# Kernel tuning notes

Measured on AMD Instinct MI355X. Metric: run time of the kernel, lower is better.

## Reference

```python
import jax, jax.numpy as jnp
import numpy as np

N_NODES = 100000


def _graph_conv(x, W, b, src, dst, norm):
    # DGL GraphConv(norm='left'): scale source features by 1/out_degree,
    # aggregate (sum over incoming edges). in_feats > out_feats so weight
    # multiply happens before aggregation (mathematically equivalent either way).
    h = x @ W  # [N, out]
    msg = (h * norm[:, None])[src]  # gather per-edge messages [E, out]
    agg = jax.ops.segment_sum(msg, dst, num_segments=N_NODES)
    return agg + b


def setup_inputs() -> dict:
    key = jax.random.key(0)
    ks = jax.random.split(key, 10)
    in_f, hid_f, out_f = 256, 128, 64
    n_edges = 1_600_000
    feat = jax.random.normal(ks[0], (N_NODES, in_f), dtype=jnp.float32)
    src = jax.random.randint(ks[1], (n_edges,), 0, N_NODES, dtype=jnp.int32)
    dst = jax.random.randint(ks[2], (n_edges,), 0, N_NODES, dtype=jnp.int32)
    noise = jax.random.normal(ks[3], (N_NODES, out_f), dtype=jnp.float32)
    s1 = 1.0 / np.sqrt(in_f)
    s2 = 1.0 / np.sqrt(hid_f)
    W_shared = jax.random.uniform(ks[4], (in_f, hid_f), minval=-s1, maxval=s1, dtype=jnp.float32)
    b_shared = jnp.zeros((hid_f,), jnp.float32)
    W_mu = jax.random.uniform(ks[5], (hid_f, out_f), minval=-s2, maxval=s2, dtype=jnp.float32)
    b_mu = jnp.zeros((out_f,), jnp.float32)
    W_ls = jax.random.uniform(ks[6], (hid_f, out_f), minval=-s2, maxval=s2, dtype=jnp.float32)
    b_ls = jnp.zeros((out_f,), jnp.float32)
    return {"feat": feat, "W_shared": W_shared, "b_shared": b_shared,
            "W_mu": W_mu, "b_mu": b_mu, "W_ls": W_ls, "b_ls": b_ls,
            "noise": noise, "src": src, "dst": dst}


def reference(feat, W_shared, b_shared, W_mu, b_mu, W_ls, b_ls, noise, src, dst):
    # left-norm: 1 / out_degree (clamped to >= 1, as DGL does)
    deg_out = jax.ops.segment_sum(jnp.ones_like(src, jnp.float32), src,
                                  num_segments=N_NODES)
    norm = 1.0 / jnp.maximum(deg_out, 1.0)
    # shared first GraphConv with ReLU activation
    h = jax.nn.relu(_graph_conv(feat, W_shared, b_shared, src, dst, norm))
    # two heads (no activation)
    mu = _graph_conv(h, W_mu, b_mu, src, dst, norm)
    log_sigma = _graph_conv(h, W_ls, b_ls, src, dst, norm)
    # reparameterized sample
    return mu + noise * jnp.exp(log_sigma)
```

## Files before the change

### kernel.cpp

```cpp
#include <hip/hip_runtime.h>
#include <hip/hip_bf16.h>
#include <math.h>

typedef __attribute__((ext_vector_type(8))) short short8;
typedef __attribute__((ext_vector_type(4))) float f32x4;

__device__ __forceinline__ unsigned short f2bf(float f) {
    unsigned int u = __float_as_uint(f);
    u += 0x7FFF + ((u >> 16) & 1);
    return (unsigned short)(u >> 16);
}
__device__ __forceinline__ float b2f(unsigned short s) {
    return __uint_as_float(((unsigned int)s) << 16);
}
__device__ __forceinline__ unsigned int f2bf2(float a, float b) {
    __hip_bfloat162 h = __float22bfloat162_rn(make_float2(a, b));
    return *(unsigned int*)&h;
}
__device__ __forceinline__ void gl_lds16(const void* g, void* l) {
    __builtin_amdgcn_global_load_lds(
        (const __attribute__((address_space(1))) void*)g,
        (__attribute__((address_space(3))) void*)l, 16, 0, 0);
}

#define EB 2048
#define SH 9
#define BSZ 512

__global__ __launch_bounds__(256)
void k1_hist(const int* __restrict__ src, const int* __restrict__ dst,
             int* __restrict__ bhist, int E, int NB2) {
    __shared__ int hist[512];
    int t = threadIdx.x;
    int NB = NB2 >> 1;
    for (int i = t; i < NB2; i += 256) hist[i] = 0;
    __syncthreads();
    int base = blockIdx.x * EB;
    int end = min(base + EB, E);
    for (int e = base + 4 * t; e < end; e += 1024) {
        if (e + 3 < end) {
            int4 d4 = *(const int4*)&dst[e];
            int4 s4 = *(const int4*)&src[e];
            atomicAdd(&hist[d4.x >> SH], 1);
            atomicAdd(&hist[d4.y >> SH], 1);
            atomicAdd(&hist[d4.z >> SH], 1);
            atomicAdd(&hist[d4.w >> SH], 1);
            atomicAdd(&hist[NB + (s4.x >> SH)], 1);
            atomicAdd(&hist[NB + (s4.y >> SH)], 1);
            atomicAdd(&hist[NB + (s4.z >> SH)], 1);
            atomicAdd(&hist[NB + (s4.w >> SH)], 1);
        } else {
            for (int q = e; q < end; ++q) {
                atomicAdd(&hist[dst[q] >> SH], 1);
                atomicAdd(&hist[NB + (src[q] >> SH)], 1);
            }
        }
    }
    __syncthreads();
    for (int i = t; i < NB2; i += 256)
        bhist[(size_t)blockIdx.x * NB2 + i] = hist[i];
}

__global__ __launch_bounds__(512)
void kc1_totals(const int* __restrict__ bhist, int* __restrict__ totals,
                int PB, int NB2) {
    int t = threadIdx.x;
    if (t >= NB2) return;
    int slice = (PB + 15) / 16;
    int b0 = blockIdx.x * slice;
    int b1 = min(b0 + slice, PB);
    int s = 0;
    for (int blk = b0; blk < b1; ++blk) s += bhist[(size_t)blk * NB2 + t];
    if (s) atomicAdd(&totals[t], s);
}

__global__ __launch_bounds__(512)
void kc2_scan(const int* __restrict__ totals, int* __restrict__ bbase, int NB) {
    __shared__ int s[512];
    int t = threadIdx.x;
    int half = t >> 8;
    int idx = t & 255;
    int v = (idx < NB) ? totals[half * NB + idx] : 0;
    s[t] = v;
    __syncthreads();
    for (int off = 1; off < 256; off <<= 1) {
        int u = (idx >= off) ? s[t - off] : 0;
        __syncthreads();
        s[t] += u;
        __syncthreads();
    }
    if (idx < NB) bbase[half * NB + idx] = s[t] - v;
}

__global__ __launch_bounds__(1024)
void kc3_boff(const int* __restrict__ bhist, const int* __restrict__ bbase,
              int* __restrict__ boffT, int PB, int NB2) {
    __shared__ int sums[1024];
    int b = blockIdx.x;
    int t = threadIdx.x;
    int v = (t < PB) ? bhist[(size_t)t * NB2 + b] : 0;
    sums[t] = v;
    __syncthreads();
    for (int off = 1; off < 1024; off <<= 1) {
        int u = (t >= off) ? sums[t - off] : 0;
        __syncthreads();
        sums[t] += u;
        __syncthreads();
    }
    if (t < PB) boffT[(size_t)b * PB + t] = bbase[b] + sums[t] - v;
}

__global__ __launch_bounds__(256)
void k2_scatter(const int* __restrict__ src, const int* __restrict__ dst,
                const int* __restrict__ boffT, int* __restrict__ parr,
                unsigned short* __restrict__ sarr, int E, int PB, int NB2) {
    __shared__ int cnt[512];
    int t = threadIdx.x;
    int blk = blockIdx.x;
    int NB = NB2 >> 1;
    for (int i = t; i < NB2; i += 256) cnt[i] = boffT[(size_t)i * PB + blk];
    __syncthreads();
    int base = blk * EB;
    int end = min(base + EB, E);
    for (int e = base + 4 * t; e < end; e += 1024) {
        if (e + 3 < end) {
            int4 s4 = *(const int4*)&src[e];
            int4 d4 = *(const int4*)&dst[e];
            int p0 = atomicAdd(&cnt[d4.x >> SH], 1);
            parr[p0] = (s4.x << SH) | (d4.x & (BSZ - 1));
            int p1 = atomicAdd(&cnt[d4.y >> SH], 1);
            parr[p1] = (s4.y << SH) | (d4.y & (BSZ - 1));
            int p2 = atomicAdd(&cnt[d4.z >> SH], 1);
            parr[p2] = (s4.z << SH) | (d4.z & (BSZ - 1));
            int p3 = atomicAdd(&cnt[d4.w >> SH], 1);
            parr[p3] = (s4.w << SH) | (d4.w & (BSZ - 1));
            int q0 = atomicAdd(&cnt[NB + (s4.x >> SH)], 1);
            sarr[q0] = (unsigned short)(s4.x & (BSZ - 1));
            int q1 = atomicAdd(&cnt[NB + (s4.y >> SH)], 1);
            sarr[q1] = (unsigned short)(s4.y & (BSZ - 1));
            int q2 = atomicAdd(&cnt[NB + (s4.z >> SH)], 1);
            sarr[q2] = (unsigned short)(s4.z & (BSZ - 1));
            int q3 = atomicAdd(&cnt[NB + (s4.w >> SH)], 1);
            sarr[q3] = (unsigned short)(s4.w & (BSZ - 1));
        } else {
            for (int q = e; q < end; ++q) {
                int sv = src[q], dv = dst[q];
                int pd = atomicAdd(&cnt[dv >> SH], 1);
                parr[pd] = (sv << SH) | (dv & (BSZ - 1));
                int ps = atomicAdd(&cnt[NB + (sv >> SH)], 1);
                sarr[ps] = (unsigned short)(sv & (BSZ - 1));
            }
        }
    }
}

__global__ __launch_bounds__(1024)
void k3_dst(const int* __restrict__ parr, const int* __restrict__ totals,
            const int* __restrict__ bbase, int* __restrict__ row_off,
            int* __restrict__ col, int N, int E) {
    __shared__ int hist[512], sc[512];
    int b = blockIdx.x, t = threadIdx.x;
    if (b == 0 && t == 0) row_off[N] = E;
    int ne = totals[b];
    int ebase = bbase[b];
    if (t < 512) hist[t] = 0;
    __syncthreads();
    for (int i = t; i < ne; i += 1024)
        atomicAdd(&hist[parr[ebase + i] & (BSZ - 1)], 1);
    __syncthreads();
    int h = 0;
    if (t < 512) { h = hist[t]; sc[t] = h; }
    __syncthreads();
    for (int off = 1; off < 512; off <<= 1) {
        int u = (t < 512 && t >= off) ? sc[t - off] : 0;
        __syncthreads();
        if (t < 512) sc[t] += u;
        __syncthreads();
    }
    if (t < 512) {
        int excl = sc[t] - h;
        int node = b * BSZ + t;
        if (node < N) row_off[node] = ebase + excl;
        hist[t] = ebase + excl;
    }
    __syncthreads();
    for (int i = t; i < ne; i += 1024) {
        int pr = parr[ebase + i];
        int slot = atomicAdd(&hist[pr & (BSZ - 1)], 1);
        col[slot] = pr >> SH;
    }
}

__global__ __launch_bounds__(1024)
void k3_src(const unsigned short* __restrict__ sarr, const int* __restrict__ totals_s,
            const int* __restrict__ bbase_s, float* __restrict__ norm, int N) {
    __shared__ int hist[512];
    int b = blockIdx.x, t = threadIdx.x;
    int ne = totals_s[b];
    int sb = bbase_s[b];
    if (t < 512) hist[t] = 0;
    __syncthreads();
    for (int i = t; i < ne; i += 1024)
        atomicAdd(&hist[sarr[sb + i]], 1);
    __syncthreads();
    int node = b * BSZ + t;
    if (t < 512 && node < N) {
        int d = hist[t];
        norm[node] = 1.0f / (float)(d > 1 ? d : 1);
    }
}


__global__ __launch_bounds__(256)
void k_wprep(const float* __restrict__ Wsh, const float* __restrict__ Wmu,
             const float* __restrict__ Wls, unsigned short* __restrict__ W1T,
             unsigned short* __restrict__ W2T) {
    int b = blockIdx.x, t = threadIdx.x;
    if (b < 128) {
        W1T[(size_t)b * 256 + t] = f2bf(Wsh[(size_t)t * 128 + b]);
    } else {
        int n = b - 128;
        if (t < 128) {
            float v = (n < 64) ? Wmu[(size_t)t * 64 + n]
                               : Wls[(size_t)t * 64 + (n - 64)];
            W2T[(size_t)n * 128 + t] = f2bf(v);
        }
    }
}

__global__ __launch_bounds__(256)
void k_gemm1(const float* __restrict__ A, int M,
             const unsigned short* __restrict__ W1T,
             const float* __restrict__ norm, unsigned short* __restrict__ outb) {
    __shared__ char ldsA[64 * 1040];
    const int w = threadIdx.x >> 6;
    const int lane = threadIdx.x & 63;
    const int quad = lane >> 4;
    const int l16 = lane & 15;
    const int cl = w * 16 + l16;
    const int r0 = blockIdx.x * 64;

#pragma unroll
    for (int i = 0; i < 16; ++i) {
        int row = r0 + w * 16 + i;
        if (row >= M) row = M - 1;
        const char* g = (const char*)A + (size_t)row * 1024 + lane * 16;
        char* l = ldsA + (w * 16 + i) * 1040 + lane * 16;
        gl_lds16(g, l);
    }

    short8 bw[2][8];
#pragma unroll
    for (int hf = 0; hf < 2; ++hf) {
        const unsigned short* wp = W1T + (size_t)(hf * 64 + cl) * 256 + quad * 8;
#pragma unroll
        for (int ks = 0; ks < 8; ++ks)
            bw[hf][ks] = *(const short8*)(wp + ks * 32);
    }
    __syncthreads();

    f32x4 acc[4][2];
#pragma unroll
    for (int m = 0; m < 4; ++m) {
        acc[m][0] = (f32x4){0.f, 0.f, 0.f, 0.f};
        acc[m][1] = (f32x4){0.f, 0.f, 0.f, 0.f};
    }
#pragma unroll
    for (int ks = 0; ks < 8; ++ks) {
#pragma unroll
        for (int m = 0; m < 4; ++m) {
            const float* pr = (const float*)(ldsA + (m * 16 + l16) * 1040 +
                                             (ks * 32 + quad * 8) * 4);
            float4 x = *(const float4*)pr;
            float4 y = *(const float4*)(pr + 4);
            union { short8 v; unsigned int u[4]; } c;
            c.u[0] = f2bf2(x.x, x.y);
            c.u[1] = f2bf2(x.z, x.w);
            c.u[2] = f2bf2(y.x, y.y);
            c.u[3] = f2bf2(y.z, y.w);
            acc[m][0] = __builtin_amdgcn_mfma_f32_16x16x32_bf16(bw[0][ks], c.v, acc[m][0], 0, 0, 0);
            acc[m][1] = __builtin_amdgcn_mfma_f32_16x16x32_bf16(bw[1][ks], c.v, acc[m][1], 0, 0, 0);
        }
    }
    const int colbase = w * 16 + quad * 4;
#pragma unroll
    for (int m = 0; m < 4; ++m) {
        int row = r0 + m * 16 + l16;
        if (row < M) {
            float nm = norm[row];
            ushort4 o0, o1;
            o0.x = f2bf(acc[m][0][0] * nm); o0.y = f2bf(acc[m][0][1] * nm);
            o0.z = f2bf(acc[m][0][2] * nm); o0.w = f2bf(acc[m][0][3] * nm);
            o1.x = f2bf(acc[m][1][0] * nm); o1.y = f2bf(acc[m][1][1] * nm);
            o1.z = f2bf(acc[m][1][2] * nm); o1.w = f2bf(acc[m][1][3] * nm);
            *(ushort4*)&outb[(size_t)row * 128 + colbase] = o0;
            *(ushort4*)&outb[(size_t)row * 128 + 64 + colbase] = o1;
        }
    }
}

__global__ __launch_bounds__(256)
void k_gemm2(const unsigned short* __restrict__ A, int M,
             const unsigned short* __restrict__ W2T,
             const float* __restrict__ norm, unsigned short* __restrict__ outb) {
    __shared__ char ldsB[16 * 1040];
    const int w = threadIdx.x >> 6;
    const int lane = threadIdx.x & 63;
    const int quad = lane >> 4;
    const int l16 = lane & 15;
    const int cl = w * 16 + l16;
    const int r0 = blockIdx.x * 64;

#pragma unroll
    for (int i = 0; i < 4; ++i) {
        int c = w * 4 + i;
        int crow = r0 + c * 4;
        if (crow + 4 > M) crow = M - 4;
        const char* g = (const char*)A + (size_t)crow * 256 + lane * 16;
        char* l = ldsB + c * 1040 + lane * 16;
        gl_lds16(g, l);
    }

    short8 bw[2][4];
#pragma unroll
    for (int hf = 0; hf < 2; ++hf) {
        const unsigned short* wp = W2T + (size_t)(hf * 64 + cl) * 128 + quad * 8;
#pragma unroll
        for (int ks = 0; ks < 4; ++ks)
            bw[hf][ks] = *(const short8*)(wp + ks * 32);
    }
    __syncthreads();

    f32x4 acc[4][2];
#pragma unroll
    for (int m = 0; m < 4; ++m) {
        acc[m][0] = (f32x4){0.f, 0.f, 0.f, 0.f};
        acc[m][1] = (f32x4){0.f, 0.f, 0.f, 0.f};
    }
#pragma unroll
    for (int ks = 0; ks < 4; ++ks) {
#pragma unroll
        for (int m = 0; m < 4; ++m) {
            int row = m * 16 + l16;
            short8 af = *(const short8*)(ldsB + (row >> 2) * 1040 + (row & 3) * 256 +
                                         (ks * 32 + quad * 8) * 2);
            acc[m][0] = __builtin_amdgcn_mfma_f32_16x16x32_bf16(bw[0][ks], af, acc[m][0], 0, 0, 0);
            acc[m][1] = __builtin_amdgcn_mfma_f32_16x16x32_bf16(bw[1][ks], af, acc[m][1], 0, 0, 0);
        }
    }
    const int colbase = w * 16 + quad * 4;
#pragma unroll
    for (int m = 0; m < 4; ++m) {
        int row = r0 + m * 16 + l16;
        if (row < M) {
            float nm = norm[row];
            ushort4 o0, o1;
            o0.x = f2bf(acc[m][0][0] * nm); o0.y = f2bf(acc[m][0][1] * nm);
            o0.z = f2bf(acc[m][0][2] * nm); o0.w = f2bf(acc[m][0][3] * nm);
            o1.x = f2bf(acc[m][1][0] * nm); o1.y = f2bf(acc[m][1][1] * nm);
            o1.z = f2bf(acc[m][1][2] * nm); o1.w = f2bf(acc[m][1][3] * nm);
            *(ushort4*)&outb[(size_t)row * 128 + colbase] = o0;
            *(ushort4*)&outb[(size_t)row * 128 + 64 + colbase] = o1;
        }
    }
}

__global__ __launch_bounds__(256)
void k_spmm_relu(const int* __restrict__ row_off, const int* __restrict__ col,
                 const unsigned short* __restrict__ hxb, const float* __restrict__ bias,
                 unsigned short* __restrict__ hb, int N) {
    int g = (blockIdx.x * blockDim.x + threadIdx.x) >> 5;
    int l = threadIdx.x & 31;
    if (g >= N) return;
    int e0 = row_off[g], e1 = row_off[g + 1];
    const ushort4* base = (const ushort4*)hxb;
    float4 acc = make_float4(0.f, 0.f, 0.f, 0.f);
    int e = e0;
    for (; e + 7 < e1; e += 8) {
        ushort4 v0 = base[(size_t)col[e] * 32 + l];
        ushort4 v1 = base[(size_t)col[e + 1] * 32 + l];
        ushort4 v2 = base[(size_t)col[e + 2] * 32 + l];
        ushort4 v3 = base[(size_t)col[e + 3] * 32 + l];
        ushort4 v4 = base[(size_t)col[e + 4] * 32 + l];
        ushort4 v5 = base[(size_t)col[e + 5] * 32 + l];
        ushort4 v6 = base[(size_t)col[e + 6] * 32 + l];
        ushort4 v7 = base[(size_t)col[e + 7] * 32 + l];
        acc.x += ((b2f(v0.x) + b2f(v1.x)) + (b2f(v2.x) + b2f(v3.x))) +
                 ((b2f(v4.x) + b2f(v5.x)) + (b2f(v6.x) + b2f(v7.x)));
        acc.y += ((b2f(v0.y) + b2f(v1.y)) + (b2f(v2.y) + b2f(v3.y))) +
                 ((b2f(v4.y) + b2f(v5.y)) + (b2f(v6.y) + b2f(v7.y)));
        acc.z += ((b2f(v0.z) + b2f(v1.z)) + (b2f(v2.z) + b2f(v3.z))) +
                 ((b2f(v4.z) + b2f(v5.z)) + (b2f(v6.z) + b2f(v7.z)));
        acc.w += ((b2f(v0.w) + b2f(v1.w)) + (b2f(v2.w) + b2f(v3.w))) +
                 ((b2f(v4.w) + b2f(v5.w)) + (b2f(v6.w) + b2f(v7.w)));
    }
    for (; e + 1 < e1; e += 2) {
        ushort4 a = base[(size_t)col[e] * 32 + l];
        ushort4 b = base[(size_t)col[e + 1] * 32 + l];
        acc.x += b2f(a.x) + b2f(b.x);
        acc.y += b2f(a.y) + b2f(b.y);
        acc.z += b2f(a.z) + b2f(b.z);
        acc.w += b2f(a.w) + b2f(b.w);
    }
    if (e < e1) {
        ushort4 a = base[(size_t)col[e] * 32 + l];
        acc.x += b2f(a.x); acc.y += b2f(a.y); acc.z += b2f(a.z); acc.w += b2f(a.w);
    }
    float4 bi = ((const float4*)bias)[l];
    ushort4 r;
    r.x = f2bf(fmaxf(acc.x + bi.x, 0.f));
    r.y = f2bf(fmaxf(acc.y + bi.y, 0.f));
    r.z = f2bf(fmaxf(acc.z + bi.z, 0.f));
    r.w = f2bf(fmaxf(acc.w + bi.w, 0.f));
    ((ushort4*)hb)[(size_t)g * 32 + l] = r;
}

__global__ __launch_bounds__(256)
void k_spmm_out(const int* __restrict__ row_off, const int* __restrict__ col,
                const unsigned short* __restrict__ hcb, const float* __restrict__ bmu,
                const float* __restrict__ bls, const float* __restrict__ noise,
                float* __restrict__ out, int N) {
    int g = (blockIdx.x * blockDim.x + threadIdx.x) >> 5;
    int l = threadIdx.x & 31;
    if (g >= N) return;
    int e0 = row_off[g], e1 = row_off[g + 1];
    const ushort4* base = (const ushort4*)hcb;
    float4 acc = make_float4(0.f, 0.f, 0.f, 0.f);
    int e = e0;
    for (; e + 7 < e1; e += 8) {
        ushort4 v0 = base[(size_t)col[e] * 32 + l];
        ushort4 v1 = base[(size_t)col[e + 1] * 32 + l];
        ushort4 v2 = base[(size_t)col[e + 2] * 32 + l];
        ushort4 v3 = base[(size_t)col[e + 3] * 32 + l];
        ushort4 v4 = base[(size_t)col[e + 4] * 32 + l];
        ushort4 v5 = base[(size_t)col[e + 5] * 32 + l];
        ushort4 v6 = base[(size_t)col[e + 6] * 32 + l];
        ushort4 v7 = base[(size_t)col[e + 7] * 32 + l];
        acc.x += ((b2f(v0.x) + b2f(v1.x)) + (b2f(v2.x) + b2f(v3.x))) +
                 ((b2f(v4.x) + b2f(v5.x)) + (b2f(v6.x) + b2f(v7.x)));
        acc.y += ((b2f(v0.y) + b2f(v1.y)) + (b2f(v2.y) + b2f(v3.y))) +
                 ((b2f(v4.y) + b2f(v5.y)) + (b2f(v6.y) + b2f(v7.y)));
        acc.z += ((b2f(v0.z) + b2f(v1.z)) + (b2f(v2.z) + b2f(v3.z))) +
                 ((b2f(v4.z) + b2f(v5.z)) + (b2f(v6.z) + b2f(v7.z)));
        acc.w += ((b2f(v0.w) + b2f(v1.w)) + (b2f(v2.w) + b2f(v3.w))) +
                 ((b2f(v4.w) + b2f(v5.w)) + (b2f(v6.w) + b2f(v7.w)));
    }
    for (; e + 1 < e1; e += 2) {
        ushort4 a = base[(size_t)col[e] * 32 + l];
        ushort4 b = base[(size_t)col[e + 1] * 32 + l];
        acc.x += b2f(a.x) + b2f(b.x);
        acc.y += b2f(a.y) + b2f(b.y);
        acc.z += b2f(a.z) + b2f(b.z);
        acc.w += b2f(a.w) + b2f(b.w);
    }
    if (e < e1) {
        ushort4 a = base[(size_t)col[e] * 32 + l];
        acc.x += b2f(a.x); acc.y += b2f(a.y); acc.z += b2f(a.z); acc.w += b2f(a.w);
    }
    int lane64 = threadIdx.x & 63;
    int p = (lane64 + 16) & 63;
    float lx = __shfl(acc.x, p, 64);
    float ly = __shfl(acc.y, p, 64);
    float lz = __shfl(acc.z, p, 64);
    float lw = __shfl(acc.w, p, 64);
    if (l < 16) {
        float4 bm = ((const float4*)bmu)[l];
        float4 bl = ((const float4*)bls)[l];
        float4 nz = ((const float4*)noise)[(size_t)g * 16 + l];
        float4 o;
        o.x = (acc.x + bm.x) + nz.x * expf(lx + bl.x);
        o.y = (acc.y + bm.y) + nz.y * expf(ly + bl.y);
        o.z = (acc.z + bm.z) + nz.z * expf(lz + bl.z);
        o.w = (acc.w + bm.w) + nz.w * expf(lw + bl.w);
        ((float4*)out)[(size_t)g * 16 + l] = o;
    }
}

static inline char* align64(char* p) {
    return (char*)(((uintptr_t)p + 63) & ~(uintptr_t)63);
}

extern "C" void kernel_launch(void* const* d_in, const int* in_sizes, int n_in,
                              void* d_out, int out_size, void* d_ws, size_t ws_size,
                              hipStream_t stream) {
    const float* feat  = (const float*)d_in[0];
    const float* Wsh   = (const float*)d_in[1];
    const float* bsh   = (const float*)d_in[2];
    const float* Wmu   = (const float*)d_in[3];
    const float* bmu   = (const float*)d_in[4];
    const float* Wls   = (const float*)d_in[5];
    const float* bls   = (const float*)d_in[6];
    const float* noise = (const float*)d_in[7];
    const int*   src   = (const int*)d_in[8];
    const int*   dst   = (const int*)d_in[9];
    float* out = (float*)d_out;

    const int N = in_sizes[0] / 256;
    const int E = in_sizes[8];
    const int PB = (E + EB - 1) / EB;
    const int NB = (N + BSZ - 1) / BSZ;
    const int NB2 = 2 * NB;

    char* p = (char*)d_ws;
    float* norm   = (float*)p;                  p += (size_t)N * 4;          p = align64(p);
    int* row_off  = (int*)p;                    p += (size_t)(N + 4) * 4;    p = align64(p);
    int* totals   = (int*)p;                    p += 512 * 4;
    int* bbase    = (int*)p;                    p += 512 * 4;                p = align64(p);
    unsigned short* W1T = (unsigned short*)p;   p += (size_t)128 * 256 * 2;
    unsigned short* W2T = (unsigned short*)p;   p += (size_t)128 * 128 * 2;
    p = align64(p);
    int* bhist    = (int*)p;                    p += (size_t)PB * NB2 * 4;   p = align64(p);
    int* boffT    = (int*)p;                    p += (size_t)NB2 * PB * 4;   p = align64(p);
    int* parr     = (int*)p;                    p += (size_t)E * 4;
    unsigned short* sarr = (unsigned short*)p;  p += (size_t)E * 2;          p = align64(p);
    int* col      = (int*)p;                    p += (size_t)E * 4;          p = align64(p);
    unsigned short* hxb = (unsigned short*)p;
    unsigned short* hb  = (unsigned short*)d_out;

    hipMemsetAsync(totals, 0, 512 * sizeof(int), stream);
    k_wprep<<<256, 256, 0, stream>>>(Wsh, Wmu, Wls, W1T, W2T);
    k1_hist<<<PB, 256, 0, stream>>>(src, dst, bhist, E, NB2);
    kc1_totals<<<16, 512, 0, stream>>>(bhist, totals, PB, NB2);
    kc2_scan<<<1, 512, 0, stream>>>(totals, bbase, NB);
    kc3_boff<<<NB2, 1024, 0, stream>>>(bhist, bbase, boffT, PB, NB2);
    k2_scatter<<<PB, 256, 0, stream>>>(src, dst, boffT, parr, sarr, E, PB, NB2);
    k3_dst<<<NB, 1024, 0, stream>>>(parr, totals, bbase, row_off, col, N, E);
    k3_src<<<NB, 1024, 0, stream>>>(sarr, totals + NB, bbase + NB, norm, N);

    int gtiles = (N + 63) / 64;
    k_gemm1<<<gtiles, 256, 0, stream>>>(feat, N, W1T, norm, hxb);
    k_spmm_relu<<<(N * 32 + 255) / 256, 256, 0, stream>>>(row_off, col, hxb, bsh, hb, N);
    k_gemm2<<<gtiles, 256, 0, stream>>>(hb, N, W2T, norm, hxb);
    k_spmm_out<<<(N * 32 + 255) / 256, 256, 0, stream>>>(row_off, col, hxb, bmu, bls, noise, out, N);
}
```

Baseline: 444.6 us.

## Fuse second aggregation with head GEMM and merge CSR build kernels

The second-layer pipeline changes order: the norm scaling moves into the ReLU aggregation, and a new fused kernel gathers neighbor rows of the normalized hidden features into LDS, then multiplies by the stacked head weights with MFMA and applies the reparameterization epilogue. This drops the separate GEMM2 pass and the round trip of its output through memory, at the cost of aggregating 128-wide rows instead of projecting first. Separately, the scan kernel and memset are folded into existing kernels (redundant per-block scans of the totals), and the dst/src CSR finalization kernels are merged into one launch. A fallback path keeps the old three-kernel sequence when the workspace is too small.

```diff
diff --git a/kernel.cpp b/kernel.cpp
--- a/kernel.cpp
+++ b/kernel.cpp
@@ -74,30 +74,24 @@
     if (s) atomicAdd(&totals[t], s);
 }
 
-__global__ __launch_bounds__(512)
-void kc2_scan(const int* __restrict__ totals, int* __restrict__ bbase, int NB) {
-    __shared__ int s[512];
-    int t = threadIdx.x;
-    int half = t >> 8;
-    int idx = t & 255;
-    int v = (idx < NB) ? totals[half * NB + idx] : 0;
-    s[t] = v;
-    __syncthreads();
-    for (int off = 1; off < 256; off <<= 1) {
-        int u = (idx >= off) ? s[t - off] : 0;
-        __syncthreads();
-        s[t] += u;
-        __syncthreads();
-    }
-    if (idx < NB) bbase[half * NB + idx] = s[t] - v;
-}
-
 __global__ __launch_bounds__(1024)
-void kc3_boff(const int* __restrict__ bhist, const int* __restrict__ bbase,
-              int* __restrict__ boffT, int PB, int NB2) {
+void kc3_boff(const int* __restrict__ bhist, const int* __restrict__ totals,
+              int* __restrict__ boffT, int PB, int NB) {
     __shared__ int sums[1024];
+    __shared__ int tb[512];
     int b = blockIdx.x;
     int t = threadIdx.x;
+    int NB2 = 2 * NB;
+    if (t < 512) tb[t] = (t < NB2) ? totals[t] : 0;
+    __syncthreads();
+    for (int off = 1; off < 512; off <<= 1) {
+        int u = (t < 512 && t >= off) ? tb[t - off] : 0;
+        __syncthreads();
+        if (t < 512) tb[t] += u;
+        __syncthreads();
+    }
+    int lo = (b < NB) ? 0 : NB;
+    int base = ((b > lo) ? tb[b - 1] : 0) - ((lo > 0 && b > lo) ? tb[lo - 1] : 0);
     int v = (t < PB) ? bhist[(size_t)t * NB2 + b] : 0;
     sums[t] = v;
     __syncthreads();
@@ -107,7 +101,7 @@
         sums[t] += u;
         __syncthreads();
     }
-    if (t < PB) boffT[(size_t)b * PB + t] = bbase[b] + sums[t] - v;
+    if (t < PB) boffT[(size_t)b * PB + t] = base + sums[t] - v;
 }
 
 __global__ __launch_bounds__(256)
@@ -155,58 +149,66 @@
 }
 
 __global__ __launch_bounds__(1024)
-void k3_dst(const int* __restrict__ parr, const int* __restrict__ totals,
-            const int* __restrict__ bbase, int* __restrict__ row_off,
-            int* __restrict__ col, int N, int E) {
+void k3_both(const int* __restrict__ parr, const unsigned short* __restrict__ sarr,
+             const int* __restrict__ totals, int* __restrict__ row_off,
+             int* __restrict__ col, float* __restrict__ norm,
+             int N, int E, int NB) {
     __shared__ int hist[512], sc[512];
+    __shared__ int tb[512];
     int b = blockIdx.x, t = threadIdx.x;
-    if (b == 0 && t == 0) row_off[N] = E;
-    int ne = totals[b];
-    int ebase = bbase[b];
-    if (t < 512) hist[t] = 0;
-    __syncthreads();
-    for (int i = t; i < ne; i += 1024)
-        atomicAdd(&hist[parr[ebase + i] & (BSZ - 1)], 1);
-    __syncthreads();
-    int h = 0;
-    if (t < 512) { h = hist[t]; sc[t] = h; }
+    int NB2 = 2 * NB;
+    if (t < 512) tb[t] = (t < NB2) ? totals[t] : 0;
     __syncthreads();
     for (int off = 1; off < 512; off <<= 1) {
-        int u = (t < 512 && t >= off) ? sc[t - off] : 0;
-        __syncthreads();
-        if (t < 512) sc[t] += u;
-        __syncthreads();
-    }
-    if (t < 512) {
-        int excl = sc[t] - h;
-        int node = b * BSZ + t;
-        if (node < N) row_off[node] = ebase + excl;
-        hist[t] = ebase + excl;
-    }
-    __syncthreads();
-    for (int i = t; i < ne; i += 1024) {
-        int pr = parr[ebase + i];
-        int slot = atomicAdd(&hist[pr & (BSZ - 1)], 1);
-        col[slot] = pr >> SH;
-    }
-}
-
-__global__ __launch_bounds__(1024)
-void k3_src(const unsigned short* __restrict__ sarr, const int* __restrict__ totals_s,
-            const int* __restrict__ bbase_s, float* __restrict__ norm, int N) {
-    __shared__ int hist[512];
-    int b = blockIdx.x, t = threadIdx.x;
-    int ne = totals_s[b];
-    int sb = bbase_s[b];
-    if (t < 512) hist[t] = 0;
-    __syncthreads();
-    for (int i = t; i < ne; i += 1024)
-        atomicAdd(&hist[sarr[sb + i]], 1);
-    __syncthreads();
-    int node = b * BSZ + t;
-    if (t < 512 && node < N) {
-        int d = hist[t];
-        norm[node] = 1.0f / (float)(d > 1 ? d : 1);
+        int u = (t < 512 && t >= off) ? tb[t - off] : 0;
+        __syncthreads();
+        if (t < 512) tb[t] += u;
+        __syncthreads();
+    }
+    if (b < NB) {
+        if (b == 0 && t == 0) row_off[N] = E;
+        int ne = totals[b];
+        int ebase = (b > 0) ? tb[b - 1] : 0;
+        if (t < 512) hist[t] = 0;
+        __syncthreads();
+        for (int i = t; i < ne; i += 1024)
+            atomicAdd(&hist[parr[ebase + i] & (BSZ - 1)], 1);
+        __syncthreads();
+        int h = 0;
+        if (t < 512) { h = hist[t]; sc[t] = h; }
+        __syncthreads();
+        for (int off = 1; off < 512; off <<= 1) {
+            int u = (t < 512 && t >= off) ? sc[t - off] : 0;
+            __syncthreads();
+            if (t < 512) sc[t] += u;
+            __syncthreads();
+        }
+        if (t < 512) {
+            int excl = sc[t] - h;
+            int node = b * BSZ + t;
+            if (node < N) row_off[node] = ebase + excl;
+            hist[t] = ebase + excl;
+        }
+        __syncthreads();
+        for (int i = t; i < ne; i += 1024) {
+            int pr = parr[ebase + i];
+            int slot = atomicAdd(&hist[pr & (BSZ - 1)], 1);
+            col[slot] = pr >> SH;
+        }
+    } else {
+        int bs = b - NB;
+        int ne = totals[NB + bs];
+        int sbase = (bs > 0) ? (tb[b - 1] - tb[NB - 1]) : 0;
+        if (t < 512) hist[t] = 0;
+        __syncthreads();
+        for (int i = t; i < ne; i += 1024)
+            atomicAdd(&hist[sarr[sbase + i]], 1);
+        __syncthreads();
+        int node = bs * BSZ + t;
+        if (t < 512 && node < N) {
+            int d = hist[t];
+            norm[node] = 1.0f / (float)(d > 1 ? d : 1);
+        }
     }
 }
 
@@ -214,8 +216,9 @@
 __global__ __launch_bounds__(256)
 void k_wprep(const float* __restrict__ Wsh, const float* __restrict__ Wmu,
              const float* __restrict__ Wls, unsigned short* __restrict__ W1T,
-             unsigned short* __restrict__ W2T) {
+             unsigned short* __restrict__ W2T, int* __restrict__ totals) {
     int b = blockIdx.x, t = threadIdx.x;
+    if (b == 0) { totals[t] = 0; totals[256 + t] = 0; }
     if (b < 128) {
         W1T[(size_t)b * 256 + t] = f2bf(Wsh[(size_t)t * 128 + b]);
     } else {
@@ -299,81 +302,11 @@
     }
 }
 
-__global__ __launch_bounds__(256)
-void k_gemm2(const unsigned short* __restrict__ A, int M,
-             const unsigned short* __restrict__ W2T,
-             const float* __restrict__ norm, unsigned short* __restrict__ outb) {
-    __shared__ char ldsB[16 * 1040];
-    const int w = threadIdx.x >> 6;
-    const int lane = threadIdx.x & 63;
-    const int quad = lane >> 4;
-    const int l16 = lane & 15;
-    const int cl = w * 16 + l16;
-    const int r0 = blockIdx.x * 64;
-
-#pragma unroll
-    for (int i = 0; i < 4; ++i) {
-        int c = w * 4 + i;
-        int crow = r0 + c * 4;
-        if (crow + 4 > M) crow = M - 4;
-        const char* g = (const char*)A + (size_t)crow * 256 + lane * 16;
-        char* l = ldsB + c * 1040 + lane * 16;
-        gl_lds16(g, l);
-    }
-
-    short8 bw[2][4];
-#pragma unroll
-    for (int hf = 0; hf < 2; ++hf) {
-        const unsigned short* wp = W2T + (size_t)(hf * 64 + cl) * 128 + quad * 8;
-#pragma unroll
-        for (int ks = 0; ks < 4; ++ks)
-            bw[hf][ks] = *(const short8*)(wp + ks * 32);
-    }
-    __syncthreads();
-
-    f32x4 acc[4][2];
-#pragma unroll
-    for (int m = 0; m < 4; ++m) {
-        acc[m][0] = (f32x4){0.f, 0.f, 0.f, 0.f};
-        acc[m][1] = (f32x4){0.f, 0.f, 0.f, 0.f};
-    }
-#pragma unroll
-    for (int ks = 0; ks < 4; ++ks) {
-#pragma unroll
-        for (int m = 0; m < 4; ++m) {
-            int row = m * 16 + l16;
-            short8 af = *(const short8*)(ldsB + (row >> 2) * 1040 + (row & 3) * 256 +
-                                         (ks * 32 + quad * 8) * 2);
-            acc[m][0] = __builtin_amdgcn_mfma_f32_16x16x32_bf16(bw[0][ks], af, acc[m][0], 0, 0, 0);
-            acc[m][1] = __builtin_amdgcn_mfma_f32_16x16x32_bf16(bw[1][ks], af, acc[m][1], 0, 0, 0);
-        }
-    }
-    const int colbase = w * 16 + quad * 4;
-#pragma unroll
-    for (int m = 0; m < 4; ++m) {
-        int row = r0 + m * 16 + l16;
-        if (row < M) {
-            float nm = norm[row];
-            ushort4 o0, o1;
-            o0.x = f2bf(acc[m][0][0] * nm); o0.y = f2bf(acc[m][0][1] * nm);
-            o0.z = f2bf(acc[m][0][2] * nm); o0.w = f2bf(acc[m][0][3] * nm);
-            o1.x = f2bf(acc[m][1][0] * nm); o1.y = f2bf(acc[m][1][1] * nm);
-            o1.z = f2bf(acc[m][1][2] * nm); o1.w = f2bf(acc[m][1][3] * nm);
-            *(ushort4*)&outb[(size_t)row * 128 + colbase] = o0;
-            *(ushort4*)&outb[(size_t)row * 128 + 64 + colbase] = o1;
-        }
-    }
-}
-
-__global__ __launch_bounds__(256)
-void k_spmm_relu(const int* __restrict__ row_off, const int* __restrict__ col,
-                 const unsigned short* __restrict__ hxb, const float* __restrict__ bias,
-                 unsigned short* __restrict__ hb, int N) {
-    int g = (blockIdx.x * blockDim.x + threadIdx.x) >> 5;
-    int l = threadIdx.x & 31;
-    if (g >= N) return;
+__device__ __forceinline__ float4 gather_row(const int* __restrict__ row_off,
+                                             const int* __restrict__ col,
+                                             const ushort4* __restrict__ base,
+                                             int g, int l) {
     int e0 = row_off[g], e1 = row_off[g + 1];
-    const ushort4* base = (const ushort4*)hxb;
     float4 acc = make_float4(0.f, 0.f, 0.f, 0.f);
     int e = e0;
     for (; e + 7 < e1; e += 8) {
@@ -406,13 +339,160 @@
         ushort4 a = base[(size_t)col[e] * 32 + l];
         acc.x += b2f(a.x); acc.y += b2f(a.y); acc.z += b2f(a.z); acc.w += b2f(a.w);
     }
+    return acc;
+}
+
+__global__ __launch_bounds__(256)
+void k_spmm_relu(const int* __restrict__ row_off, const int* __restrict__ col,
+                 const unsigned short* __restrict__ hxb, const float* __restrict__ bias,
+                 const float* __restrict__ norm, unsigned short* __restrict__ hb, int N) {
+    int g = (blockIdx.x * blockDim.x + threadIdx.x) >> 5;
+    int l = threadIdx.x & 31;
+    if (g >= N) return;
+    float4 acc = gather_row(row_off, col, (const ushort4*)hxb, g, l);
     float4 bi = ((const float4*)bias)[l];
+    float nm = norm[g];
     ushort4 r;
-    r.x = f2bf(fmaxf(acc.x + bi.x, 0.f));
-    r.y = f2bf(fmaxf(acc.y + bi.y, 0.f));
-    r.z = f2bf(fmaxf(acc.z + bi.z, 0.f));
-    r.w = f2bf(fmaxf(acc.w + bi.w, 0.f));
+    r.x = f2bf(fmaxf(acc.x + bi.x, 0.f) * nm);
+    r.y = f2bf(fmaxf(acc.y + bi.y, 0.f) * nm);
+    r.z = f2bf(fmaxf(acc.z + bi.z, 0.f) * nm);
+    r.w = f2bf(fmaxf(acc.w + bi.w, 0.f) * nm);
     ((ushort4*)hb)[(size_t)g * 32 + l] = r;
+}
+
+__global__ __launch_bounds__(512)
+void k_spmm_gemm_out(const int* __restrict__ row_off, const int* __restrict__ col,
+                     const unsigned short* __restrict__ hnb,
+                     const unsigned short* __restrict__ W2T,
+                     const float* __restrict__ bmu, const float* __restrict__ bls,
+                     const float* __restrict__ noise, float* __restrict__ out, int N) {
+    __shared__ char ldsB[16 * 1040];
+    const int tid = threadIdx.x;
+    const int r0 = blockIdx.x * 64;
+    const int hw = tid >> 5;
+    const int l = tid & 31;
+    const ushort4* base = (const ushort4*)hnb;
+#pragma unroll
+    for (int it = 0; it < 4; ++it) {
+        int lrow = hw + 16 * it;
+        int g = r0 + lrow;
+        float4 acc = make_float4(0.f, 0.f, 0.f, 0.f);
+        if (g < N) acc = gather_row(row_off, col, base, g, l);
+        ushort4 r;
+        r.x = f2bf(acc.x); r.y = f2bf(acc.y); r.z = f2bf(acc.z); r.w = f2bf(acc.w);
+        *(ushort4*)(ldsB + (lrow >> 2) * 1040 + (lrow & 3) * 256 + l * 8) = r;
+    }
+    const int w = tid >> 6;
+    const int lane = tid & 63;
+    const int quad = lane >> 4;
+    const int l16 = lane & 15;
+    const int wcol = w & 3;
+    const int mb = (w >> 2) * 2;
+    const int cl = wcol * 16 + l16;
+    short8 bw[2][4];
+#pragma unroll
+    for (int hf = 0; hf < 2; ++hf) {
+        const unsigned short* wp = W2T + (size_t)(hf * 64 + cl) * 128 + quad * 8;
+#pragma unroll
+        for (int ks = 0; ks < 4; ++ks)
+            bw[hf][ks] = *(const short8*)(wp + ks * 32);
+    }
+    __syncthreads();
+    f32x4 acc2[2][2];
+#pragma unroll
+    for (int mi = 0; mi < 2; ++mi) {
+        acc2[mi][0] = (f32x4){0.f, 0.f, 0.f, 0.f};
+        acc2[mi][1] = (f32x4){0.f, 0.f, 0.f, 0.f};
+    }
+#pragma unroll
+    for (int ks = 0; ks < 4; ++ks) {
+#pragma unroll
+        for (int mi = 0; mi < 2; ++mi) {
+            int row = (mb + mi) * 16 + l16;
+            short8 af = *(const short8*)(ldsB + (row >> 2) * 1040 + (row & 3) * 256 +
+                                         (ks * 32 + quad * 8) * 2);
+            acc2[mi][0] = __builtin_amdgcn_mfma_f32_16x16x32_bf16(bw[0][ks], af, acc2[mi][0], 0, 0, 0);
+            acc2[mi][1] = __builtin_amdgcn_mfma_f32_16x16x32_bf16(bw[1][ks], af, acc2[mi][1], 0, 0, 0);
+        }
+    }
+    const int colbase = wcol * 16 + quad * 4;
+    float4 bm = ((const float4*)bmu)[colbase >> 2];
+    float4 bl = ((const float4*)bls)[colbase >> 2];
+#pragma unroll
+    for (int mi = 0; mi < 2; ++mi) {
+        int row = r0 + (mb + mi) * 16 + l16;
+        if (row < N) {
+            float4 nz = ((const float4*)noise)[(size_t)row * 16 + (colbase >> 2)];
+            float4 o;
+            o.x = (acc2[mi][0][0] + bm.x) + nz.x * expf(acc2[mi][1][0] + bl.x);
+            o.y = (acc2[mi][0][1] + bm.y) + nz.y * expf(acc2[mi][1][1] + bl.y);
+            o.z = (acc2[mi][0][2] + bm.z) + nz.z * expf(acc2[mi][1][2] + bl.z);
+            o.w = (acc2[mi][0][3] + bm.w) + nz.w * expf(acc2[mi][1][3] + bl.w);
+            ((float4*)out)[(size_t)row * 16 + (colbase >> 2)] = o;
+        }
+    }
+}
+
+__global__ __launch_bounds__(256)
+void k_gemm2(const unsigned short* __restrict__ A, int M,
+             const unsigned short* __restrict__ W2T,
+             unsigned short* __restrict__ outb) {
+    __shared__ char ldsB[16 * 1040];
+    const int w = threadIdx.x >> 6;
+    const int lane = threadIdx.x & 63;
+    const int quad = lane >> 4;
+    const int l16 = lane & 15;
+    const int cl = w * 16 + l16;
+    const int r0 = blockIdx.x * 64;
+#pragma unroll
+    for (int i = 0; i < 4; ++i) {
+        int c = w * 4 + i;
+        int crow = r0 + c * 4;
+        if (crow + 4 > M) crow = M - 4;
+        const char* g = (const char*)A + (size_t)crow * 256 + lane * 16;
+        char* l = ldsB + c * 1040 + lane * 16;
+        gl_lds16(g, l);
+    }
+    short8 bw[2][4];
+#pragma unroll
+    for (int hf = 0; hf < 2; ++hf) {
+        const unsigned short* wp = W2T + (size_t)(hf * 64 + cl) * 128 + quad * 8;
+#pragma unroll
+        for (int ks = 0; ks < 4; ++ks)
+            bw[hf][ks] = *(const short8*)(wp + ks * 32);
+    }
+    __syncthreads();
+    f32x4 acc[4][2];
+#pragma unroll
+    for (int m = 0; m < 4; ++m) {
+        acc[m][0] = (f32x4){0.f, 0.f, 0.f, 0.f};
+        acc[m][1] = (f32x4){0.f, 0.f, 0.f, 0.f};
+    }
+#pragma unroll
+    for (int ks = 0; ks < 4; ++ks) {
+#pragma unroll
+        for (int m = 0; m < 4; ++m) {
+            int row = m * 16 + l16;
+            short8 af = *(const short8*)(ldsB + (row >> 2) * 1040 + (row & 3) * 256 +
+                                         (ks * 32 + quad * 8) * 2);
+            acc[m][0] = __builtin_amdgcn_mfma_f32_16x16x32_bf16(bw[0][ks], af, acc[m][0], 0, 0, 0);
+            acc[m][1] = __builtin_amdgcn_mfma_f32_16x16x32_bf16(bw[1][ks], af, acc[m][1], 0, 0, 0);
+        }
+    }
+    const int colbase = w * 16 + quad * 4;
+#pragma unroll
+    for (int m = 0; m < 4; ++m) {
+        int row = r0 + m * 16 + l16;
+        if (row < M) {
+            ushort4 o0, o1;
+            o0.x = f2bf(acc[m][0][0]); o0.y = f2bf(acc[m][0][1]);
+            o0.z = f2bf(acc[m][0][2]); o0.w = f2bf(acc[m][0][3]);
+            o1.x = f2bf(acc[m][1][0]); o1.y = f2bf(acc[m][1][1]);
+            o1.z = f2bf(acc[m][1][2]); o1.w = f2bf(acc[m][1][3]);
+            *(ushort4*)&outb[(size_t)row * 128 + colbase] = o0;
+            *(ushort4*)&outb[(size_t)row * 128 + 64 + colbase] = o1;
+        }
+    }
 }
 
 __global__ __launch_bounds__(256)
@@ -423,40 +503,7 @@
     int g = (blockIdx.x * blockDim.x + threadIdx.x) >> 5;
     int l = threadIdx.x & 31;
     if (g >= N) return;
-    int e0 = row_off[g], e1 = row_off[g + 1];
-    const ushort4* base = (const ushort4*)hcb;
-    float4 acc = make_float4(0.f, 0.f, 0.f, 0.f);
-    int e = e0;
-    for (; e + 7 < e1; e += 8) {
-        ushort4 v0 = base[(size_t)col[e] * 32 + l];
-        ushort4 v1 = base[(size_t)col[e + 1] * 32 + l];
-        ushort4 v2 = base[(size_t)col[e + 2] * 32 + l];
-        ushort4 v3 = base[(size_t)col[e + 3] * 32 + l];
-        ushort4 v4 = base[(size_t)col[e + 4] * 32 + l];
-        ushort4 v5 = base[(size_t)col[e + 5] * 32 + l];
-        ushort4 v6 = base[(size_t)col[e + 6] * 32 + l];
-        ushort4 v7 = base[(size_t)col[e + 7] * 32 + l];
-        acc.x += ((b2f(v0.x) + b2f(v1.x)) + (b2f(v2.x) + b2f(v3.x))) +
-                 ((b2f(v4.x) + b2f(v5.x)) + (b2f(v6.x) + b2f(v7.x)));
-        acc.y += ((b2f(v0.y) + b2f(v1.y)) + (b2f(v2.y) + b2f(v3.y))) +
-                 ((b2f(v4.y) + b2f(v5.y)) + (b2f(v6.y) + b2f(v7.y)));
-        acc.z += ((b2f(v0.z) + b2f(v1.z)) + (b2f(v2.z) + b2f(v3.z))) +
-                 ((b2f(v4.z) + b2f(v5.z)) + (b2f(v6.z) + b2f(v7.z)));
-        acc.w += ((b2f(v0.w) + b2f(v1.w)) + (b2f(v2.w) + b2f(v3.w))) +
-                 ((b2f(v4.w) + b2f(v5.w)) + (b2f(v6.w) + b2f(v7.w)));
-    }
-    for (; e + 1 < e1; e += 2) {
-        ushort4 a = base[(size_t)col[e] * 32 + l];
-        ushort4 b = base[(size_t)col[e + 1] * 32 + l];
-        acc.x += b2f(a.x) + b2f(b.x);
-        acc.y += b2f(a.y) + b2f(b.y);
-        acc.z += b2f(a.z) + b2f(b.z);
-        acc.w += b2f(a.w) + b2f(b.w);
-    }
-    if (e < e1) {
-        ushort4 a = base[(size_t)col[e] * 32 + l];
-        acc.x += b2f(a.x); acc.y += b2f(a.y); acc.z += b2f(a.z); acc.w += b2f(a.w);
-    }
+    float4 acc = gather_row(row_off, col, (const ushort4*)hcb, g, l);
     int lane64 = threadIdx.x & 63;
     int p = (lane64 + 16) & 63;
     float lx = __shfl(acc.x, p, 64);
@@ -504,8 +551,7 @@
     char* p = (char*)d_ws;
     float* norm   = (float*)p;                  p += (size_t)N * 4;          p = align64(p);
     int* row_off  = (int*)p;                    p += (size_t)(N + 4) * 4;    p = align64(p);
-    int* totals   = (int*)p;                    p += 512 * 4;
-    int* bbase    = (int*)p;                    p += 512 * 4;                p = align64(p);
+    int* totals   = (int*)p;                    p += 512 * 4;                p = align64(p);
     unsigned short* W1T = (unsigned short*)p;   p += (size_t)128 * 256 * 2;
     unsigned short* W2T = (unsigned short*)p;   p += (size_t)128 * 128 * 2;
     p = align64(p);
@@ -514,22 +560,27 @@
     int* parr     = (int*)p;                    p += (size_t)E * 4;
     unsigned short* sarr = (unsigned short*)p;  p += (size_t)E * 2;          p = align64(p);
     int* col      = (int*)p;                    p += (size_t)E * 4;          p = align64(p);
-    unsigned short* hxb = (unsigned short*)p;
-    unsigned short* hb  = (unsigned short*)d_out;
-
-    hipMemsetAsync(totals, 0, 512 * sizeof(int), stream);
-    k_wprep<<<256, 256, 0, stream>>>(Wsh, Wmu, Wls, W1T, W2T);
+    unsigned short* hxb = (unsigned short*)p;   p += (size_t)N * 128 * 2;    p = align64(p);
+    unsigned short* hnb = (unsigned short*)p;
+    size_t need_fused = (size_t)((p + (size_t)N * 128 * 2) - (char*)d_ws);
+    bool fused = (need_fused <= ws_size);
+
+    k_wprep<<<256, 256, 0, stream>>>(Wsh, Wmu, Wls, W1T, W2T, totals);
     k1_hist<<<PB, 256, 0, stream>>>(src, dst, bhist, E, NB2);
     kc1_totals<<<16, 512, 0, stream>>>(bhist, totals, PB, NB2);
-    kc2_scan<<<1, 512, 0, stream>>>(totals, bbase, NB);
-    kc3_boff<<<NB2, 1024, 0, stream>>>(bhist, bbase, boffT, PB, NB2);
+    kc3_boff<<<NB2, 1024, 0, stream>>>(bhist, totals, boffT, PB, NB);
     k2_scatter<<<PB, 256, 0, stream>>>(src, dst, boffT, parr, sarr, E, PB, NB2);
-    k3_dst<<<NB, 1024, 0, stream>>>(parr, totals, bbase, row_off, col, N, E);
-    k3_src<<<NB, 1024, 0, stream>>>(sarr, totals + NB, bbase + NB, norm, N);
+    k3_both<<<NB2, 1024, 0, stream>>>(parr, sarr, totals, row_off, col, norm, N, E, NB);
 
     int gtiles = (N + 63) / 64;
     k_gemm1<<<gtiles, 256, 0, stream>>>(feat, N, W1T, norm, hxb);
-    k_spmm_relu<<<(N * 32 + 255) / 256, 256, 0, stream>>>(row_off, col, hxb, bsh, hb, N);
-    k_gemm2<<<gtiles, 256, 0, stream>>>(hb, N, W2T, norm, hxb);
-    k_spmm_out<<<(N * 32 + 255) / 256, 256, 0, stream>>>(row_off, col, hxb, bmu, bls, noise, out, N);
-}
+    if (fused) {
+        k_spmm_relu<<<(N * 32 + 255) / 256, 256, 0, stream>>>(row_off, col, hxb, bsh, norm, hnb, N);
+        k_spmm_gemm_out<<<gtiles, 512, 0, stream>>>(row_off, col, hnb, W2T, bmu, bls, noise, out, N);
+    } else {
+        unsigned short* hb = (unsigned short*)d_out;
+        k_spmm_relu<<<(N * 32 + 255) / 256, 256, 0, stream>>>(row_off, col, hxb, bsh, norm, hb, N);
+        k_gemm2<<<gtiles, 256, 0, stream>>>(hb, N, W2T, hxb);
+        k_spmm_out<<<(N * 32 + 255) / 256, 256, 0, stream>>>(row_off, col, hxb, bmu, bls, noise, out, N);
+    }
+}
```

After: 433.4 us. 2.5% less time.
